# Optimization experiments

Hardware: AMD Instinct MI355X
Metric: run time of the kernel (lower is better)

## Reference

```python
import jax, jax.numpy as jnp
import numpy as np

N_HEADS = 16
D_HEAD = 64
D_MODEL = 1024


def setup_inputs() -> dict:
    key = jax.random.key(0)
    k_x, k_q, k_k, k_v, k_o = jax.random.split(key, 5)
    std = 1.0 / np.sqrt(D_MODEL)
    B, T = 4, 2048
    return {
        "x": jax.random.normal(k_x, (B, T, D_MODEL), dtype=jnp.float32),
        "W_Q": jax.random.normal(k_q, (D_MODEL, N_HEADS * D_HEAD), dtype=jnp.float32) * std,
        "W_K": jax.random.normal(k_k, (D_MODEL, N_HEADS * D_HEAD), dtype=jnp.float32) * std,
        "W_V": jax.random.normal(k_v, (D_MODEL, N_HEADS * D_HEAD), dtype=jnp.float32) * std,
        "W_O": jax.random.normal(k_o, (N_HEADS * D_HEAD, D_MODEL), dtype=jnp.float32) * std,
    }


def reference(x, W_Q, W_K, W_V, W_O):
    B, T, _ = x.shape
    H, D = N_HEADS, D_HEAD
    # projections: [B,T,H,D]
    q = (x @ W_Q).reshape(B, T, H, D)
    k = (x @ W_K).reshape(B, T, H, D)
    v = (x @ W_V).reshape(B, T, H, D)
    scale = 1.0 / jnp.sqrt(jnp.asarray(D, dtype=x.dtype))
    # scores: [B,H,T,T]
    scores = jnp.einsum("bqhd,bkhd->bhqk", q, k) * scale
    causal = jnp.tril(jnp.ones((T, T), dtype=bool))
    scores = jnp.where(causal[None, None], scores, jnp.asarray(-jnp.inf, dtype=scores.dtype))
    attn = jax.nn.softmax(scores, axis=-1)
    out = jnp.einsum("bhqk,bkhd->bqhd", attn, v).reshape(B, T, H * D)
    return out @ W_O
```

## Files before the change

kernel.cpp:

```cpp
#include <hip/hip_runtime.h>

typedef unsigned short u16;
typedef short bf16x8 __attribute__((ext_vector_type(8)));
typedef float f32x4 __attribute__((ext_vector_type(4)));

__device__ inline u16 f32_to_bf16(float f) {
  union { float f; unsigned int u; } v; v.f = f;
  unsigned int r = v.u + 0x7FFFu + ((v.u >> 16) & 1u);
  return (u16)(r >> 16);
}

__device__ inline float red16_sum(float x) {
#pragma unroll
  for (int m = 8; m >= 1; m >>= 1) x += __shfl_xor(x, m);
  return x;
}

__global__ __launch_bounds__(256) void xcvt_kernel(const float* __restrict__ in,
                                                   u16* __restrict__ out) {
  size_t i = (size_t)blockIdx.x * 256 + threadIdx.x;
  float4 f0 = ((const float4*)in)[2 * i];
  float4 f1 = ((const float4*)in)[2 * i + 1];
  union { u16 t[8]; uint4 v; } pk;
  pk.t[0] = f32_to_bf16(f0.x); pk.t[1] = f32_to_bf16(f0.y);
  pk.t[2] = f32_to_bf16(f0.z); pk.t[3] = f32_to_bf16(f0.w);
  pk.t[4] = f32_to_bf16(f1.x); pk.t[5] = f32_to_bf16(f1.y);
  pk.t[6] = f32_to_bf16(f1.z); pk.t[7] = f32_to_bf16(f1.w);
  ((uint4*)out)[i] = pk.v;
}

__global__ __launch_bounds__(256) void transpose_cvt_kernel(const float* __restrict__ in,
                                                            u16* __restrict__ out) {
  __shared__ __align__(16) float tile[32][33];
  const int tx = threadIdx.x & 31, ty = threadIdx.x >> 5;
  const int bx = blockIdx.x * 32, by = blockIdx.y * 32;
#pragma unroll
  for (int i = 0; i < 32; i += 8)
    tile[ty + i][tx] = in[(size_t)(by + ty + i) * 1024 + bx + tx];
  __syncthreads();
#pragma unroll
  for (int i = 0; i < 32; i += 8)
    out[(size_t)(bx + ty + i) * 1024 + by + tx] = f32_to_bf16(tile[tx][ty + i]);
}

#define LDP 40

template <int MODE, int OUTF32>
__global__ __launch_bounds__(256) void gemm_kernel(const u16* __restrict__ A,
                                                   const u16* __restrict__ Bt,
                                                   void* __restrict__ Craw) {
  const int N = 1024, K = 1024;
  __shared__ __align__(16) u16 sA[128 * LDP];
  __shared__ __align__(16) u16 sB[128 * LDP];

  const int tid = threadIdx.x;
  const int lane = tid & 63, wave = tid >> 6;
  const int quad = lane >> 4, l16 = lane & 15;
  const int bn = blockIdx.x, bm = blockIdx.y;
  const int m0 = bm * 128, n0 = bn * 128;
  const int wm = (wave >> 1) * 64, wn = (wave & 1) * 64;

  f32x4 acc[4][4] = {};

  for (int k0 = 0; k0 < K; k0 += 32) {
    __syncthreads();
#pragma unroll
    for (int i = 0; i < 2; ++i) {
      int c = tid + 256 * i;
      int row = c >> 2;
      int col = (c & 3) * 8;
      *(uint4*)(sA + row * LDP + col) =
          *(const uint4*)(A + (size_t)(m0 + row) * K + k0 + col);
      *(uint4*)(sB + row * LDP + col) =
          *(const uint4*)(Bt + (size_t)(n0 + row) * K + k0 + col);
    }
    __syncthreads();

    bf16x8 afr[4], bfr[4];
#pragma unroll
    for (int mt = 0; mt < 4; ++mt)
      afr[mt] = *(const bf16x8*)(sA + (wm + mt * 16 + l16) * LDP + quad * 8);
#pragma unroll
    for (int nt = 0; nt < 4; ++nt)
      bfr[nt] = *(const bf16x8*)(sB + (wn + nt * 16 + l16) * LDP + quad * 8);
#pragma unroll
    for (int mt = 0; mt < 4; ++mt)
#pragma unroll
      for (int nt = 0; nt < 4; ++nt)
        acc[mt][nt] = __builtin_amdgcn_mfma_f32_16x16x32_bf16(afr[mt], bfr[nt],
                                                              acc[mt][nt], 0, 0, 0);
  }

#pragma unroll
  for (int mt = 0; mt < 4; ++mt) {
#pragma unroll
    for (int nt = 0; nt < 4; ++nt) {
#pragma unroll
      for (int r = 0; r < 4; ++r) {
        int mrow = m0 + wm + mt * 16 + quad * 4 + r;
        int ncol = n0 + wn + nt * 16 + l16;
        float fv = acc[mt][nt][r];
        if (OUTF32) {
          ((float*)Craw)[(size_t)mrow * N + ncol] = fv;
        } else if (MODE == 0) {
          ((u16*)Craw)[(size_t)mrow * N + ncol] = f32_to_bf16(fv);
        } else {
          int b = mrow >> 11, t = mrow & 2047;
          int h = ncol >> 6, d = ncol & 63;
          ((u16*)Craw)[((size_t)((b * 16 + h) * 64 + d)) * 2048 + t] = f32_to_bf16(fv);
        }
      }
    }
  }
}

#define LDS_S 72

__global__ __launch_bounds__(256, 4) void attn_kernel(const u16* __restrict__ Qm,
                                                      const u16* __restrict__ Km,
                                                      const u16* __restrict__ Vt,
                                                      u16* __restrict__ Ctx) {
  const int qt = 15 - blockIdx.x;
  const int h = blockIdx.y, b = blockIdx.z;
  const int tid = threadIdx.x, lane = tid & 63, wave = tid >> 6;
  const int quad = lane >> 4, l16 = lane & 15;
  const int qb = qt * 128;

  __shared__ __align__(16) u16 sK[64 * LDS_S];
  __shared__ __align__(16) u16 sV[64 * LDS_S];
  __shared__ __align__(16) u16 sP[4][2][16 * LDS_S];

  bf16x8 qf[2][2];
#pragma unroll
  for (int mt = 0; mt < 2; ++mt) {
    const size_t qrow = (size_t)(b * 2048 + qb + wave * 32 + mt * 16 + l16);
#pragma unroll
    for (int kk = 0; kk < 2; ++kk)
      qf[mt][kk] = *(const bf16x8*)(Qm + qrow * 1024 + h * 64 + kk * 32 + quad * 8);
  }

  f32x4 o_acc[2][4] = {};
  float ps[2][4] = {};

  const int nkt = 2 * (qt + 1);
  for (int kt = 0; kt < nkt; ++kt) {
    const int k0 = kt * 64;
    __syncthreads();
#pragma unroll
    for (int i = 0; i < 2; ++i) {
      int c = tid + 256 * i;
      int row = c >> 3, col = (c & 7) * 8;
      *(uint4*)(sK + row * LDS_S + col) =
          *(const uint4*)(Km + ((size_t)(b * 2048 + k0 + row)) * 1024 + h * 64 + col);
      *(uint4*)(sV + row * LDS_S + col) =
          *(const uint4*)(Vt + ((size_t)((b * 16 + h) * 64 + row)) * 2048 + k0 + col);
    }
    __syncthreads();

#pragma unroll
    for (int mt = 0; mt < 2; ++mt) {
      const int qmin = qb + wave * 32 + mt * 16;
      if (k0 > qmin + 15) continue;

      f32x4 s[4];
#pragma unroll
      for (int nt = 0; nt < 4; ++nt) {
        f32x4 a = {};
#pragma unroll
        for (int kk = 0; kk < 2; ++kk) {
          bf16x8 kf = *(const bf16x8*)(sK + (nt * 16 + l16) * LDS_S + kk * 32 + quad * 8);
          a = __builtin_amdgcn_mfma_f32_16x16x32_bf16(qf[mt][kk], kf, a, 0, 0, 0);
        }
        s[nt] = a;
      }

      const bool need_mask = (k0 + 63) > qmin;
#pragma unroll
      for (int nt = 0; nt < 4; ++nt) {
#pragma unroll
        for (int r = 0; r < 4; ++r) {
          float v = s[nt][r] * 0.125f;
          if (need_mask) {
            int qi = qmin + quad * 4 + r;
            int kj = k0 + nt * 16 + l16;
            if (kj > qi) v = -1e30f;
          }
          float p = __expf(v);
          s[nt][r] = p;
          ps[mt][r] += p;
        }
      }

#pragma unroll
      for (int nt = 0; nt < 4; ++nt)
#pragma unroll
        for (int r = 0; r < 4; ++r)
          sP[wave][mt][(quad * 4 + r) * LDS_S + nt * 16 + l16] = f32_to_bf16(s[nt][r]);

#pragma unroll
      for (int kk = 0; kk < 2; ++kk) {
        bf16x8 pf = *(const bf16x8*)(sP[wave][mt] + l16 * LDS_S + kk * 32 + quad * 8);
#pragma unroll
        for (int dt = 0; dt < 4; ++dt) {
          bf16x8 vf = *(const bf16x8*)(sV + (dt * 16 + l16) * LDS_S + kk * 32 + quad * 8);
          o_acc[mt][dt] = __builtin_amdgcn_mfma_f32_16x16x32_bf16(pf, vf,
                                                                  o_acc[mt][dt], 0, 0, 0);
        }
      }
    }
  }

  float inv_l[2][4];
#pragma unroll
  for (int mt = 0; mt < 2; ++mt)
#pragma unroll
    for (int r = 0; r < 4; ++r)
      inv_l[mt][r] = 1.0f / red16_sum(ps[mt][r]);

#pragma unroll
  for (int mt = 0; mt < 2; ++mt)
#pragma unroll
    for (int dt = 0; dt < 4; ++dt)
#pragma unroll
      for (int r = 0; r < 4; ++r) {
        int trow = qb + wave * 32 + mt * 16 + quad * 4 + r;
        Ctx[((size_t)(b * 2048 + trow)) * 1024 + h * 64 + dt * 16 + l16] =
            f32_to_bf16(o_acc[mt][dt][r] * inv_l[mt][r]);
      }
}

extern "C" void kernel_launch(void* const* d_in, const int* in_sizes, int n_in,
                              void* d_out, int out_size, void* d_ws, size_t ws_size,
                              hipStream_t stream) {
  const float* x  = (const float*)d_in[0];
  const float* wq = (const float*)d_in[1];
  const float* wk = (const float*)d_in[2];
  const float* wv = (const float*)d_in[3];
  const float* wo = (const float*)d_in[4];
  u16* ws = (u16*)d_ws;

  u16* wtq = ws + 0 * (size_t)(1 << 20);
  u16* wtk = ws + 1 * (size_t)(1 << 20);
  u16* wtv = ws + 2 * (size_t)(1 << 20);
  u16* wto = ws + 3 * (size_t)(1 << 20);
  u16* Q   = ws + 4 * (size_t)(1 << 20);
  u16* K   = ws + 12 * (size_t)(1 << 20);
  u16* Vt  = ws + 20 * (size_t)(1 << 20);
  u16* Ctx = ws + 28 * (size_t)(1 << 20);
  u16* xb  = Ctx;
  float* out = (float*)d_out;

  dim3 tb(256);
  xcvt_kernel<<<dim3(4096), tb, 0, stream>>>(x, xb);
  transpose_cvt_kernel<<<dim3(32, 32), tb, 0, stream>>>(wq, wtq);
  transpose_cvt_kernel<<<dim3(32, 32), tb, 0, stream>>>(wk, wtk);
  transpose_cvt_kernel<<<dim3(32, 32), tb, 0, stream>>>(wv, wtv);
  transpose_cvt_kernel<<<dim3(32, 32), tb, 0, stream>>>(wo, wto);

  gemm_kernel<0, 0><<<dim3(8, 64), tb, 0, stream>>>(xb, wtq, Q);
  gemm_kernel<0, 0><<<dim3(8, 64), tb, 0, stream>>>(xb, wtk, K);
  gemm_kernel<1, 0><<<dim3(8, 64), tb, 0, stream>>>(xb, wtv, Vt);

  attn_kernel<<<dim3(16, 16, 4), tb, 0, stream>>>(Q, K, Vt, Ctx);

  gemm_kernel<0, 1><<<dim3(8, 64), tb, 0, stream>>>(Ctx, wto, out);
}
```

Before: 352.6 us.

## Fuse QKV GEMMs and weight transposes, balance causal attention with paired query tiles

```diff
diff --git a/kernel.cpp b/kernel.cpp
--- a/kernel.cpp
+++ b/kernel.cpp
@@ -29,8 +29,14 @@
   ((uint4*)out)[i] = pk.v;
 }
 
-__global__ __launch_bounds__(256) void transpose_cvt_kernel(const float* __restrict__ in,
-                                                            u16* __restrict__ out) {
+__global__ __launch_bounds__(256) void transpose_cvt4_kernel(const float* __restrict__ i0,
+                                                             const float* __restrict__ i1,
+                                                             const float* __restrict__ i2,
+                                                             const float* __restrict__ i3,
+                                                             u16* __restrict__ wbase) {
+  const int z = blockIdx.z;
+  const float* in = (z == 0) ? i0 : (z == 1) ? i1 : (z == 2) ? i2 : i3;
+  u16* out = wbase + (size_t)z * (1 << 20);
   __shared__ __align__(16) float tile[32][33];
   const int tx = threadIdx.x & 31, ty = threadIdx.x >> 5;
   const int bx = blockIdx.x * 32, by = blockIdx.y * 32;
@@ -45,11 +51,11 @@
 
 #define LDP 40
 
-template <int MODE, int OUTF32>
-__global__ __launch_bounds__(256) void gemm_kernel(const u16* __restrict__ A,
-                                                   const u16* __restrict__ Bt,
-                                                   void* __restrict__ Craw) {
-  const int N = 1024, K = 1024;
+__global__ __launch_bounds__(256) void gemm_qkv_kernel(const u16* __restrict__ A,
+                                                       const u16* __restrict__ Bt,
+                                                       u16* __restrict__ Q,
+                                                       u16* __restrict__ K,
+                                                       u16* __restrict__ Vt) {
   __shared__ __align__(16) u16 sA[128 * LDP];
   __shared__ __align__(16) u16 sB[128 * LDP];
 
@@ -62,7 +68,7 @@
 
   f32x4 acc[4][4] = {};
 
-  for (int k0 = 0; k0 < K; k0 += 32) {
+  for (int k0 = 0; k0 < 1024; k0 += 32) {
     __syncthreads();
 #pragma unroll
     for (int i = 0; i < 2; ++i) {
@@ -70,9 +76,9 @@
       int row = c >> 2;
       int col = (c & 3) * 8;
       *(uint4*)(sA + row * LDP + col) =
-          *(const uint4*)(A + (size_t)(m0 + row) * K + k0 + col);
+          *(const uint4*)(A + (size_t)(m0 + row) * 1024 + k0 + col);
       *(uint4*)(sB + row * LDP + col) =
-          *(const uint4*)(Bt + (size_t)(n0 + row) * K + k0 + col);
+          *(const uint4*)(Bt + (size_t)(n0 + row) * 1024 + k0 + col);
     }
     __syncthreads();
 
@@ -91,27 +97,84 @@
                                                               acc[mt][nt], 0, 0, 0);
   }
 
+  const int proj = bn >> 3;
 #pragma unroll
   for (int mt = 0; mt < 4; ++mt) {
 #pragma unroll
     for (int nt = 0; nt < 4; ++nt) {
+#pragma unroll
+      for (int r = 0; r < 4; ++r) {
+        int mrow = m0 + wm + mt * 16 + quad * 4 + r;
+        int nloc = (n0 & 1023) + wn + nt * 16 + l16;
+        u16 bv = f32_to_bf16(acc[mt][nt][r]);
+        if (proj == 0) {
+          Q[(size_t)mrow * 1024 + nloc] = bv;
+        } else if (proj == 1) {
+          K[(size_t)mrow * 1024 + nloc] = bv;
+        } else {
+          int b = mrow >> 11, t = mrow & 2047;
+          int h = nloc >> 6, d = nloc & 63;
+          Vt[((size_t)((b * 16 + h) * 64 + d)) * 2048 + t] = bv;
+        }
+      }
+    }
+  }
+}
+
+__global__ __launch_bounds__(256) void gemm_out_kernel(const u16* __restrict__ A,
+                                                       const u16* __restrict__ Bt,
+                                                       float* __restrict__ C) {
+  __shared__ __align__(16) u16 sA[128 * LDP];
+  __shared__ __align__(16) u16 sB[128 * LDP];
+
+  const int tid = threadIdx.x;
+  const int lane = tid & 63, wave = tid >> 6;
+  const int quad = lane >> 4, l16 = lane & 15;
+  const int bn = blockIdx.x, bm = blockIdx.y;
+  const int m0 = bm * 128, n0 = bn * 128;
+  const int wm = (wave >> 1) * 64, wn = (wave & 1) * 64;
+
+  f32x4 acc[4][4] = {};
+
+  for (int k0 = 0; k0 < 1024; k0 += 32) {
+    __syncthreads();
+#pragma unroll
+    for (int i = 0; i < 2; ++i) {
+      int c = tid + 256 * i;
+      int row = c >> 2;
+      int col = (c & 3) * 8;
+      *(uint4*)(sA + row * LDP + col) =
+          *(const uint4*)(A + (size_t)(m0 + row) * 1024 + k0 + col);
+      *(uint4*)(sB + row * LDP + col) =
+          *(const uint4*)(Bt + (size_t)(n0 + row) * 1024 + k0 + col);
+    }
+    __syncthreads();
+
+    bf16x8 afr[4], bfr[4];
+#pragma unroll
+    for (int mt = 0; mt < 4; ++mt)
+      afr[mt] = *(const bf16x8*)(sA + (wm + mt * 16 + l16) * LDP + quad * 8);
+#pragma unroll
+    for (int nt = 0; nt < 4; ++nt)
+      bfr[nt] = *(const bf16x8*)(sB + (wn + nt * 16 + l16) * LDP + quad * 8);
+#pragma unroll
+    for (int mt = 0; mt < 4; ++mt)
+#pragma unroll
+      for (int nt = 0; nt < 4; ++nt)
+        acc[mt][nt] = __builtin_amdgcn_mfma_f32_16x16x32_bf16(afr[mt], bfr[nt],
+                                                              acc[mt][nt], 0, 0, 0);
+  }
+
+#pragma unroll
+  for (int mt = 0; mt < 4; ++mt)
+#pragma unroll
+    for (int nt = 0; nt < 4; ++nt)
 #pragma unroll
       for (int r = 0; r < 4; ++r) {
         int mrow = m0 + wm + mt * 16 + quad * 4 + r;
         int ncol = n0 + wn + nt * 16 + l16;
-        float fv = acc[mt][nt][r];
-        if (OUTF32) {
-          ((float*)Craw)[(size_t)mrow * N + ncol] = fv;
-        } else if (MODE == 0) {
-          ((u16*)Craw)[(size_t)mrow * N + ncol] = f32_to_bf16(fv);
-        } else {
-          int b = mrow >> 11, t = mrow & 2047;
-          int h = ncol >> 6, d = ncol & 63;
-          ((u16*)Craw)[((size_t)((b * 16 + h) * 64 + d)) * 2048 + t] = f32_to_bf16(fv);
-        }
-      }
-    }
-  }
+        C[(size_t)mrow * 1024 + ncol] = acc[mt][nt][r];
+      }
 }
 
 #define LDS_S 72
@@ -120,11 +183,11 @@
                                                       const u16* __restrict__ Km,
                                                       const u16* __restrict__ Vt,
                                                       u16* __restrict__ Ctx) {
-  const int qt = 15 - blockIdx.x;
+  const int pi = blockIdx.x;
   const int h = blockIdx.y, b = blockIdx.z;
   const int tid = threadIdx.x, lane = tid & 63, wave = tid >> 6;
   const int quad = lane >> 4, l16 = lane & 15;
-  const int qb = qt * 128;
+  const int q64[2] = {pi, 31 - pi};
 
   __shared__ __align__(16) u16 sK[64 * LDS_S];
   __shared__ __align__(16) u16 sV[64 * LDS_S];
@@ -132,17 +195,17 @@
 
   bf16x8 qf[2][2];
 #pragma unroll
-  for (int mt = 0; mt < 2; ++mt) {
-    const size_t qrow = (size_t)(b * 2048 + qb + wave * 32 + mt * 16 + l16);
+  for (int s = 0; s < 2; ++s) {
+    const size_t qrow = (size_t)(b * 2048 + q64[s] * 64 + wave * 16 + l16);
 #pragma unroll
     for (int kk = 0; kk < 2; ++kk)
-      qf[mt][kk] = *(const bf16x8*)(Qm + qrow * 1024 + h * 64 + kk * 32 + quad * 8);
+      qf[s][kk] = *(const bf16x8*)(Qm + qrow * 1024 + h * 64 + kk * 32 + quad * 8);
   }
 
   f32x4 o_acc[2][4] = {};
   float ps[2][4] = {};
 
-  const int nkt = 2 * (qt + 1);
+  const int nkt = 32 - pi;
   for (int kt = 0; kt < nkt; ++kt) {
     const int k0 = kt * 64;
     __syncthreads();
@@ -158,20 +221,20 @@
     __syncthreads();
 
 #pragma unroll
-    for (int mt = 0; mt < 2; ++mt) {
-      const int qmin = qb + wave * 32 + mt * 16;
+    for (int s = 0; s < 2; ++s) {
+      const int qmin = q64[s] * 64 + wave * 16;
       if (k0 > qmin + 15) continue;
 
-      f32x4 s[4];
+      f32x4 sc[4];
 #pragma unroll
       for (int nt = 0; nt < 4; ++nt) {
         f32x4 a = {};
 #pragma unroll
         for (int kk = 0; kk < 2; ++kk) {
           bf16x8 kf = *(const bf16x8*)(sK + (nt * 16 + l16) * LDS_S + kk * 32 + quad * 8);
-          a = __builtin_amdgcn_mfma_f32_16x16x32_bf16(qf[mt][kk], kf, a, 0, 0, 0);
+          a = __builtin_amdgcn_mfma_f32_16x16x32_bf16(qf[s][kk], kf, a, 0, 0, 0);
         }
-        s[nt] = a;
+        sc[nt] = a;
       }
 
       const bool need_mask = (k0 + 63) > qmin;
@@ -179,15 +242,15 @@
       for (int nt = 0; nt < 4; ++nt) {
 #pragma unroll
         for (int r = 0; r < 4; ++r) {
-          float v = s[nt][r] * 0.125f;
+          float v = sc[nt][r] * 0.125f;
           if (need_mask) {
             int qi = qmin + quad * 4 + r;
             int kj = k0 + nt * 16 + l16;
             if (kj > qi) v = -1e30f;
           }
           float p = __expf(v);
-          s[nt][r] = p;
-          ps[mt][r] += p;
+          sc[nt][r] = p;
+          ps[s][r] += p;
         }
       }
 
@@ -195,16 +258,16 @@
       for (int nt = 0; nt < 4; ++nt)
 #pragma unroll
         for (int r = 0; r < 4; ++r)
-          sP[wave][mt][(quad * 4 + r) * LDS_S + nt * 16 + l16] = f32_to_bf16(s[nt][r]);
+          sP[wave][s][(quad * 4 + r) * LDS_S + nt * 16 + l16] = f32_to_bf16(sc[nt][r]);
 
 #pragma unroll
       for (int kk = 0; kk < 2; ++kk) {
-        bf16x8 pf = *(const bf16x8*)(sP[wave][mt] + l16 * LDS_S + kk * 32 + quad * 8);
+        bf16x8 pf = *(const bf16x8*)(sP[wave][s] + l16 * LDS_S + kk * 32 + quad * 8);
 #pragma unroll
         for (int dt = 0; dt < 4; ++dt) {
           bf16x8 vf = *(const bf16x8*)(sV + (dt * 16 + l16) * LDS_S + kk * 32 + quad * 8);
-          o_acc[mt][dt] = __builtin_amdgcn_mfma_f32_16x16x32_bf16(pf, vf,
-                                                                  o_acc[mt][dt], 0, 0, 0);
+          o_acc[s][dt] = __builtin_amdgcn_mfma_f32_16x16x32_bf16(pf, vf,
+                                                                 o_acc[s][dt], 0, 0, 0);
         }
       }
     }
@@ -212,20 +275,20 @@
 
   float inv_l[2][4];
 #pragma unroll
-  for (int mt = 0; mt < 2; ++mt)
+  for (int s = 0; s < 2; ++s)
 #pragma unroll
     for (int r = 0; r < 4; ++r)
-      inv_l[mt][r] = 1.0f / red16_sum(ps[mt][r]);
-
-#pragma unroll
-  for (int mt = 0; mt < 2; ++mt)
+      inv_l[s][r] = 1.0f / red16_sum(ps[s][r]);
+
+#pragma unroll
+  for (int s = 0; s < 2; ++s)
 #pragma unroll
     for (int dt = 0; dt < 4; ++dt)
 #pragma unroll
       for (int r = 0; r < 4; ++r) {
-        int trow = qb + wave * 32 + mt * 16 + quad * 4 + r;
+        int trow = q64[s] * 64 + wave * 16 + quad * 4 + r;
         Ctx[((size_t)(b * 2048 + trow)) * 1024 + h * 64 + dt * 16 + l16] =
-            f32_to_bf16(o_acc[mt][dt][r] * inv_l[mt][r]);
+            f32_to_bf16(o_acc[s][dt][r] * inv_l[s][r]);
       }
 }
 
@@ -239,29 +302,22 @@
   const float* wo = (const float*)d_in[4];
   u16* ws = (u16*)d_ws;
 
-  u16* wtq = ws + 0 * (size_t)(1 << 20);
-  u16* wtk = ws + 1 * (size_t)(1 << 20);
-  u16* wtv = ws + 2 * (size_t)(1 << 20);
-  u16* wto = ws + 3 * (size_t)(1 << 20);
-  u16* Q   = ws + 4 * (size_t)(1 << 20);
-  u16* K   = ws + 12 * (size_t)(1 << 20);
-  u16* Vt  = ws + 20 * (size_t)(1 << 20);
-  u16* Ctx = ws + 28 * (size_t)(1 << 20);
-  u16* xb  = Ctx;
+  u16* wtqkv = ws;
+  u16* wto  = ws + 3 * (size_t)(1 << 20);
+  u16* Q    = ws + 4 * (size_t)(1 << 20);
+  u16* K    = ws + 12 * (size_t)(1 << 20);
+  u16* Vt   = ws + 20 * (size_t)(1 << 20);
+  u16* Ctx  = ws + 28 * (size_t)(1 << 20);
+  u16* xb   = Ctx;
   float* out = (float*)d_out;
 
   dim3 tb(256);
   xcvt_kernel<<<dim3(4096), tb, 0, stream>>>(x, xb);
-  transpose_cvt_kernel<<<dim3(32, 32), tb, 0, stream>>>(wq, wtq);
-  transpose_cvt_kernel<<<dim3(32, 32), tb, 0, stream>>>(wk, wtk);
-  transpose_cvt_kernel<<<dim3(32, 32), tb, 0, stream>>>(wv, wtv);
-  transpose_cvt_kernel<<<dim3(32, 32), tb, 0, stream>>>(wo, wto);
-
-  gemm_kernel<0, 0><<<dim3(8, 64), tb, 0, stream>>>(xb, wtq, Q);
-  gemm_kernel<0, 0><<<dim3(8, 64), tb, 0, stream>>>(xb, wtk, K);
-  gemm_kernel<1, 0><<<dim3(8, 64), tb, 0, stream>>>(xb, wtv, Vt);
+  transpose_cvt4_kernel<<<dim3(32, 32, 4), tb, 0, stream>>>(wq, wk, wv, wo, ws);
+
+  gemm_qkv_kernel<<<dim3(24, 64), tb, 0, stream>>>(xb, wtqkv, Q, K, Vt);
 
   attn_kernel<<<dim3(16, 16, 4), tb, 0, stream>>>(Q, K, Vt, Ctx);
 
-  gemm_kernel<0, 1><<<dim3(8, 64), tb, 0, stream>>>(Ctx, wto, out);
-}
+  gemm_out_kernel<<<dim3(8, 64), tb, 0, stream>>>(Ctx, wto, out);
+}
```

Measured after the change: 314.5 us. -10.8%, faster.
